# Kernel optimization log

Hardware: AMD Instinct MI355X
Metric: run time of the kernel (lower is better)

## Reference

```python
import jax, jax.numpy as jnp
import numpy as np

UNITS = 256
IN_DIM = 128
BATCH = 128
SEQ = 1024


def setup_inputs() -> dict:
    key = jax.random.key(0)
    k1, k2, k3 = jax.random.split(key, 3)
    x = jax.random.normal(k1, (BATCH, SEQ, IN_DIM), jnp.float32)
    # glorot-ish scale for stability
    input_weight = jax.random.normal(k2, (IN_DIM, 7 * UNITS), jnp.float32) * 0.05
    hidden_weight = jax.random.normal(k3, (UNITS, 3 * UNITS), jnp.float32) * 0.05
    bias = jnp.zeros((3 * UNITS,), jnp.float32)
    # constant = [eye(in_dim); zeros] of shape (units, in_dim), non-trainable
    constant = jnp.concatenate(
        [jnp.eye(IN_DIM, dtype=jnp.float32),
         jnp.zeros((UNITS - IN_DIM, IN_DIM), jnp.float32)], axis=0)
    return {"x": x, "input_weight": input_weight, "hidden_weight": hidden_weight,
            "bias": bias, "constant": constant}


def reference(x, input_weight, hidden_weight, bias, constant):
    u = hidden_weight.shape[0]
    Wxr, Wxu, Wxh, dWxr, dWxu, ddWxr, ddWxu = (
        [input_weight[:, i * u:(i + 1) * u] for i in range(7)])
    Whr, Whu, Whh = [hidden_weight[:, i * u:(i + 1) * u] for i in range(3)]
    br, bu, bh = bias[:u], bias[u:2 * u], bias[2 * u:]

    B = x.shape[0]
    h0 = jnp.zeros((B, u), x.dtype)
    s0 = jnp.zeros((B, u), x.dtype)

    def step(carry, x_t):
        h, s1, s2 = carry
        # recover padded previous inputs: (b,units) @ (units,in) -> (b,in)
        x_tm1 = s1 @ constant
        x_tm2 = s2 @ constant
        d_x = x_t - x_tm1                       # 1st-order finite diff
        dd_x = x_t - 2.0 * x_tm1 + x_tm2        # 2nd-order finite diff
        r = jax.nn.sigmoid(x_t @ Wxr + d_x @ dWxr + dd_x @ ddWxr + h @ Whr + br)
        ug = jax.nn.sigmoid(x_t @ Wxu + d_x @ dWxu + dd_x @ ddWxu + h @ Whu + bu)
        cand = jnp.tanh(x_t @ Wxh + (r * h) @ Whh + bh)
        h_new = ug * h + (1.0 - ug) * cand
        new_s1 = x_t @ constant.T               # pad x_t to units dims
        new_s2 = x_tm1 @ constant.T             # pad x_tm1 to units dims
        return (h_new, new_s1, new_s2), h_new

    xs = jnp.swapaxes(x, 0, 1)                  # (T, B, in_dim)
    _, hs = jax.lax.scan(step, (h0, s0, s0), xs)
    return jnp.swapaxes(hs, 0, 1)               # (B, T, units)
```

## Files before the change

### kernel.cpp

```cpp
#include <hip/hip_runtime.h>

#define SEQL 1024
#define BATCHN 128
#define UNITS 256
#define INDIM 128
#define G3 768

typedef __attribute__((ext_vector_type(8))) short short8;
typedef __attribute__((ext_vector_type(4))) short short4v;
typedef __attribute__((ext_vector_type(4))) float floatx4;

#define NL2E  -1.4426950408889634f
#define PL2E2  2.8853900817779268f

#define HSTRIDE 272

__device__ __forceinline__ short f2bf(float f) {
  unsigned u = __float_as_uint(f);
  u += 0x7fff + ((u >> 16) & 1);
  return (short)(u >> 16);
}
__device__ __forceinline__ float bf2f(unsigned short s) {
  return __uint_as_float(((unsigned)s) << 16);
}
__device__ __forceinline__ float fexp2(float x) {
#if __has_builtin(__builtin_amdgcn_exp2f)
  return __builtin_amdgcn_exp2f(x);
#else
  return __expf(0.6931471805599453f * x);
#endif
}
__device__ __forceinline__ float frcp(float x) {
#if __has_builtin(__builtin_amdgcn_rcpf)
  return __builtin_amdgcn_rcpf(x);
#else
  return 1.f / x;
#endif
}

#define LDS_BARRIER() do {                                   \
    asm volatile("s_waitcnt lgkmcnt(0)" ::: "memory");       \
    __builtin_amdgcn_s_barrier();                            \
    asm volatile("" ::: "memory");                           \
  } while (0)

__device__ __forceinline__ void acq_spin(const int* p) {
  while (__hip_atomic_load(p, __ATOMIC_ACQUIRE, __HIP_MEMORY_SCOPE_AGENT) == 0)
    __builtin_amdgcn_s_sleep(8);
}

__global__ void prep_kernel(const float* __restrict__ iw,
                            const float* __restrict__ hw,
                            short* __restrict__ WcB, short* __restrict__ WhB,
                            int* __restrict__ flags) {
  int idx = blockIdx.x * 256 + threadIdx.x;
  const int WCN = 384 * G3;
  if (idx < WCN) {
    int k = idx / G3, n = idx % G3;
    int i = k & 127, blkk = k >> 7;
    int gsel = n >> 8, c = n & 255;
    const float* row = iw + (size_t)i * 1792;
    float v;
    if (blkk == 0) {
      v = (gsel == 0) ? row[c] + row[768 + c] + row[1280 + c]
        : (gsel == 1) ? row[256 + c] + row[1024 + c] + row[1536 + c]
                      : row[512 + c];
    } else if (blkk == 1) {
      v = (gsel == 0) ? -(row[768 + c] + 2.f * row[1280 + c])
        : (gsel == 1) ? -(row[1024 + c] + 2.f * row[1536 + c])
                      : 0.f;
    } else {
      v = (gsel == 0) ? row[1280 + c]
        : (gsel == 1) ? row[1536 + c]
                      : 0.f;
    }
    v *= (gsel == 2) ? PL2E2 : NL2E;
    int kk = k >> 5, q = (k >> 3) & 3, j = k & 7;
    WcB[(((n * 12 + kk) * 4 + q) * 8) + j] = f2bf(v);
  } else {
    idx -= WCN;
    if (idx < 256 * G3) {
      int k = idx / G3, n = idx % G3;
      float v = hw[(size_t)k * G3 + n] * ((n >> 8) == 2 ? PL2E2 : NL2E);
      int kk = k >> 5, q = (k >> 3) & 3, j = k & 7;
      WhB[(((n * 8 + kk) * 4 + q) * 8) + j] = f2bf(v);
    } else {
      idx -= 256 * G3;
      if (idx < SEQL * 8) flags[idx] = 0;
    }
  }
}

__global__ __launch_bounds__(512, 2) void fused_kernel(
    const float* __restrict__ x, const short* __restrict__ WcB,
    const float* __restrict__ bias, unsigned* __restrict__ pre2,
    const short* __restrict__ WhB, float* __restrict__ out,
    int* __restrict__ flags) {
  __shared__ __align__(16) short smem[12288];

  if (blockIdx.x >= 32) {
    const int pidx = blockIdx.x - 32;
    const int tpair = pidx >> 3, mt = pidx & 7;
    const int tid = threadIdx.x;
    const int half = tid >> 8, htid = tid & 255;
    const int t = tpair * 2 + half;
    short* xF = smem + half * 6144;

#pragma unroll
    for (int it = 0; it < 6; ++it) {
      int rr = it * 8 + (htid >> 5);
      int dt = rr >> 4, bb = rr & 15;
      int lane32 = htid & 31, c = lane32 * 4;
      floatx4 v = {0.f, 0.f, 0.f, 0.f};
      if (t >= dt)
        v = *(const floatx4*)(x + ((size_t)(mt * 16 + bb) * SEQL + (t - dt)) * INDIM + c);
      int kk = dt * 4 + (c >> 5), qq = (c >> 3) & 3, j0 = c & 7;
      short4v pk;
#pragma unroll
      for (int j = 0; j < 4; ++j) pk[j] = f2bf(v[j]);
      *(short4v*)&xF[((kk * 64 + qq * 16 + bb) * 8) + j0] = pk;
    }
    __syncthreads();

    const int wvp = htid >> 6, lane = htid & 63, ln16 = lane & 15;
    const int qp = lane >> 4;

    short8 aF[12];
#pragma unroll
    for (int kk = 0; kk < 12; ++kk) aF[kk] = *(const short8*)&xF[(kk * 64 + lane) * 8];

    unsigned* slab = pre2 + (size_t)((mt * 4 + qp) * SEQL + t) * 1536;

#pragma unroll
    for (int ig = 0; ig < 3; ++ig) {
      const int ngrp = wvp * 3 + ig;
      const float sc = (ngrp >= 8) ? PL2E2 : NL2E;
      floatx4 acc[4];
#pragma unroll
      for (int nt = 0; nt < 4; ++nt) {
        float bv = bias[ngrp * 64 + nt * 16 + ln16] * sc;
#pragma unroll
        for (int r = 0; r < 4; ++r) acc[nt][r] = bv;
      }
#pragma unroll
      for (int kk = 0; kk < 12; ++kk) {
#pragma unroll
        for (int nt = 0; nt < 4; ++nt) {
          int n = ngrp * 64 + nt * 16 + ln16;
          short8 w = *(const short8*)(WcB + (((size_t)(n * 12 + kk) * 4 + qp) * 8));
          acc[nt] = __builtin_amdgcn_mfma_f32_16x16x32_bf16(aF[kk], w, acc[nt], 0, 0, 0);
        }
      }
      const int g = ngrp >> 2;
#pragma unroll
      for (int p = 0; p < 2; ++p) {
        int wvc = (ngrp & 3) * 2 + p;
#pragma unroll
        for (int r = 0; r < 4; ++r) {
          unsigned lo = (unsigned)(unsigned short)f2bf(acc[2 * p][r]);
          unsigned hi = (unsigned)(unsigned short)f2bf(acc[2 * p + 1][r]);
          slab[g * 512 + wvc * 64 + r * 16 + ln16] = lo | (hi << 16);
        }
      }
    }

    __syncthreads();
    if (tid == 0) {
      __threadfence();
      __hip_atomic_store(&flags[(2 * tpair) * 8 + mt], 1,
                         __ATOMIC_RELEASE, __HIP_MEMORY_SCOPE_AGENT);
      __hip_atomic_store(&flags[(2 * tpair + 1) * 8 + mt], 1,
                         __ATOMIC_RELEASE, __HIP_MEMORY_SCOPE_AGENT);
    }
    return;
  }

  short* hFc = smem;
  short* rFc = smem + 4 * HSTRIDE;

  const int tid = threadIdx.x;
  const int wv = tid >> 6, lane = tid & 63, ln16 = lane & 15, q = lane >> 4;
  const int row4 = lane & 3;
  const int wg = blockIdx.x;
  const int mtg = wg >> 2;

  short8 wR[2][8], wU[2][8], wH[2][8];
#pragma unroll
  for (int nt = 0; nt < 2; ++nt) {
    int nr = wv * 32 + nt * 16 + ln16;
#pragma unroll
    for (int kk = 0; kk < 8; ++kk) {
      wR[nt][kk] = *(const short8*)(WhB + (((size_t)(nr * 8 + kk) * 4 + q) * 8));
      wU[nt][kk] = *(const short8*)(WhB + (((size_t)((256 + nr) * 8 + kk) * 4 + q) * 8));
      wH[nt][kk] = *(const short8*)(WhB + (((size_t)((512 + nr) * 8 + kk) * 4 + q) * 8));
    }
  }
  for (int i = tid; i < 4 * HSTRIDE; i += 512) { hFc[i] = 0; rFc[i] = 0; }

  const floatx4 z4 = {0.f, 0.f, 0.f, 0.f};
  float hq[2] = {0.f, 0.f};

  const unsigned* slab0 = pre2 + (size_t)wg * SEQL * 1536;

  acq_spin(&flags[0 * 8 + mtg]);
  unsigned cur0 = slab0[0 * 512 + tid];
  unsigned cur1 = slab0[1 * 512 + tid];
  unsigned cur2 = slab0[2 * 512 + tid];
  int fcur = __hip_atomic_load(&flags[1 * 8 + mtg],
                               __ATOMIC_RELAXED, __HIP_MEMORY_SCOPE_AGENT);

  float* outBase = out + ((size_t)(wg * 4 + q) * SEQL) * UNITS + wv * 32 + ln16;
  const int aoff = row4 * HSTRIDE + q * 8;
  const int woff = q * HSTRIDE + wv * 32 + ln16;

  __syncthreads();

  for (int t = 0; t < SEQL; ++t) {
    int fnxt = 1;
    if (t + 2 < SEQL)
      fnxt = __hip_atomic_load(&flags[(t + 2) * 8 + mtg],
                               __ATOMIC_RELAXED, __HIP_MEMORY_SCOPE_AGENT);
    if (t + 1 < SEQL && fcur == 0) acq_spin(&flags[(t + 1) * 8 + mtg]);
    asm volatile("" ::: "memory");

    const unsigned* nslab = slab0 + (size_t)(t < SEQL - 1 ? t + 1 : t) * 1536;
    unsigned nxt0 = nslab[0 * 512 + tid];
    unsigned nxt1 = nslab[1 * 512 + tid];
    unsigned nxt2 = nslab[2 * 512 + tid];

    floatx4 accR[2], accU[2];
    {
      const short8 a0 = *(const short8*)&hFc[aoff];
      accR[0] = __builtin_amdgcn_mfma_f32_16x16x32_bf16(a0, wR[0][0], z4, 0, 0, 0);
      accR[1] = __builtin_amdgcn_mfma_f32_16x16x32_bf16(a0, wR[1][0], z4, 0, 0, 0);
      accU[0] = __builtin_amdgcn_mfma_f32_16x16x32_bf16(a0, wU[0][0], z4, 0, 0, 0);
      accU[1] = __builtin_amdgcn_mfma_f32_16x16x32_bf16(a0, wU[1][0], z4, 0, 0, 0);
    }
#pragma unroll
    for (int kk = 1; kk < 8; ++kk) {
      const short8 a = *(const short8*)&hFc[aoff + kk * 32];
      accR[0] = __builtin_amdgcn_mfma_f32_16x16x32_bf16(a, wR[0][kk], accR[0], 0, 0, 0);
      accR[1] = __builtin_amdgcn_mfma_f32_16x16x32_bf16(a, wR[1][kk], accR[1], 0, 0, 0);
      accU[0] = __builtin_amdgcn_mfma_f32_16x16x32_bf16(a, wU[0][kk], accU[0], 0, 0, 0);
      accU[1] = __builtin_amdgcn_mfma_f32_16x16x32_bf16(a, wU[1][kk], accU[1], 0, 0, 0);
    }
    float uq[2];
#pragma unroll
    for (int nt = 0; nt < 2; ++nt) {
      float vR = (q == 0) ? accR[nt][0] : (q == 1) ? accR[nt][1]
               : (q == 2) ? accR[nt][2] : accR[nt][3];
      float vU = (q == 0) ? accU[nt][0] : (q == 1) ? accU[nt][1]
               : (q == 2) ? accU[nt][2] : accU[nt][3];
      float pR = bf2f((unsigned short)(nt ? (cur0 >> 16) : (cur0 & 0xffff)));
      float pU = bf2f((unsigned short)(nt ? (cur1 >> 16) : (cur1 & 0xffff)));
      float rg = frcp(1.f + fexp2(vR + pR));
      uq[nt]   = frcp(1.f + fexp2(vU + pU));
      rFc[woff + nt * 16] = f2bf(rg * hq[nt]);
    }
    LDS_BARRIER();

    floatx4 accH[2];
    {
      const short8 a0 = *(const short8*)&rFc[aoff];
      accH[0] = __builtin_amdgcn_mfma_f32_16x16x32_bf16(a0, wH[0][0], z4, 0, 0, 0);
      accH[1] = __builtin_amdgcn_mfma_f32_16x16x32_bf16(a0, wH[1][0], z4, 0, 0, 0);
    }
#pragma unroll
    for (int kk = 1; kk < 8; ++kk) {
      const short8 a = *(const short8*)&rFc[aoff + kk * 32];
      accH[0] = __builtin_amdgcn_mfma_f32_16x16x32_bf16(a, wH[0][kk], accH[0], 0, 0, 0);
      accH[1] = __builtin_amdgcn_mfma_f32_16x16x32_bf16(a, wH[1][kk], accH[1], 0, 0, 0);
    }
#pragma unroll
    for (int nt = 0; nt < 2; ++nt) {
      float vH = (q == 0) ? accH[nt][0] : (q == 1) ? accH[nt][1]
               : (q == 2) ? accH[nt][2] : accH[nt][3];
      float pH = bf2f((unsigned short)(nt ? (cur2 >> 16) : (cur2 & 0xffff)));
      float cand = 1.f - 2.f * frcp(1.f + fexp2(vH + pH));
      float hnew = uq[nt] * (hq[nt] - cand) + cand;
      hq[nt] = hnew;
      hFc[woff + nt * 16] = f2bf(hnew);
      outBase[(size_t)t * UNITS + nt * 16] = hnew;
    }
    cur0 = nxt0; cur1 = nxt1; cur2 = nxt2; fcur = fnxt;
    LDS_BARRIER();
  }
}

extern "C" void kernel_launch(void* const* d_in, const int* in_sizes, int n_in,
                              void* d_out, int out_size, void* d_ws, size_t ws_size,
                              hipStream_t stream) {
  const float* x    = (const float*)d_in[0];
  const float* iw   = (const float*)d_in[1];
  const float* hw   = (const float*)d_in[2];
  const float* bias = (const float*)d_in[3];
  float* out = (float*)d_out;

  unsigned* pre2 = (unsigned*)d_ws;
  const size_t preDwords = (size_t)32 * SEQL * 1536;
  short* WcB = (short*)(pre2 + preDwords);
  short* WhB = WcB + (size_t)384 * G3;
  int* flags = (int*)(WhB + (size_t)256 * G3);

  prep_kernel<<<1952, 256, 0, stream>>>(iw, hw, WcB, WhB, flags);
  fused_kernel<<<32 + 4096, 512, 0, stream>>>(x, WcB, bias, pre2, WhB, out, flags);
}
```

Before: 1.574 ms.

## Restructure input projection blocks to one timestep across all batch tiles

```diff
diff --git a/kernel.cpp b/kernel.cpp
--- a/kernel.cpp
+++ b/kernel.cpp
@@ -86,80 +86,82 @@
       WhB[(((n * 8 + kk) * 4 + q) * 8) + j] = f2bf(v);
     } else {
       idx -= 256 * G3;
-      if (idx < SEQL * 8) flags[idx] = 0;
-    }
-  }
-}
-
-__global__ __launch_bounds__(512, 2) void fused_kernel(
+      if (idx < SEQL) flags[idx] = 0;
+    }
+  }
+}
+
+__global__ __launch_bounds__(512, 1) void fused_kernel(
     const float* __restrict__ x, const short* __restrict__ WcB,
     const float* __restrict__ bias, unsigned* __restrict__ pre2,
     const short* __restrict__ WhB, float* __restrict__ out,
     int* __restrict__ flags) {
-  __shared__ __align__(16) short smem[12288];
+  __shared__ __align__(16) short xA[6144 * 8];
+  __shared__ __align__(16) short hFc[4 * HSTRIDE];
+  __shared__ __align__(16) short rFc[4 * HSTRIDE];
+
+  const int tid = threadIdx.x;
 
   if (blockIdx.x >= 32) {
-    const int pidx = blockIdx.x - 32;
-    const int tpair = pidx >> 3, mt = pidx & 7;
-    const int tid = threadIdx.x;
-    const int half = tid >> 8, htid = tid & 255;
-    const int t = tpair * 2 + half;
-    short* xF = smem + half * 6144;
-
-#pragma unroll
-    for (int it = 0; it < 6; ++it) {
-      int rr = it * 8 + (htid >> 5);
-      int dt = rr >> 4, bb = rr & 15;
-      int lane32 = htid & 31, c = lane32 * 4;
-      floatx4 v = {0.f, 0.f, 0.f, 0.f};
-      if (t >= dt)
-        v = *(const floatx4*)(x + ((size_t)(mt * 16 + bb) * SEQL + (t - dt)) * INDIM + c);
-      int kk = dt * 4 + (c >> 5), qq = (c >> 3) & 3, j0 = c & 7;
-      short4v pk;
-#pragma unroll
-      for (int j = 0; j < 4; ++j) pk[j] = f2bf(v[j]);
-      *(short4v*)&xF[((kk * 64 + qq * 16 + bb) * 8) + j0] = pk;
+    const int t = blockIdx.x - 32;
+
+#pragma unroll
+    for (int it = 0; it < 12; ++it) {
+      int u = it * 512 + tid;
+      int kk8mi = u >> 6, l6 = u & 63;
+      int kk = kk8mi >> 3, mi = kk8mi & 7;
+      int qq = l6 >> 4, bb = l6 & 15;
+      int row = mi * 16 + bb;
+      int k = kk * 32 + qq * 8;
+      int dt = k >> 7, kin = k & 127;
+      floatx4 v0 = {0.f, 0.f, 0.f, 0.f}, v1 = {0.f, 0.f, 0.f, 0.f};
+      if (t >= dt) {
+        const float* src = x + ((size_t)row * SEQL + (t - dt)) * INDIM + kin;
+        v0 = *(const floatx4*)src;
+        v1 = *(const floatx4*)(src + 4);
+      }
+      short8 pk;
+#pragma unroll
+      for (int j = 0; j < 4; ++j) { pk[j] = f2bf(v0[j]); pk[4 + j] = f2bf(v1[j]); }
+      *(short8*)&xA[u * 8] = pk;
     }
     __syncthreads();
 
-    const int wvp = htid >> 6, lane = htid & 63, ln16 = lane & 15;
-    const int qp = lane >> 4;
-
-    short8 aF[12];
-#pragma unroll
-    for (int kk = 0; kk < 12; ++kk) aF[kk] = *(const short8*)&xF[(kk * 64 + lane) * 8];
-
-    unsigned* slab = pre2 + (size_t)((mt * 4 + qp) * SEQL + t) * 1536;
-
-#pragma unroll
-    for (int ig = 0; ig < 3; ++ig) {
-      const int ngrp = wvp * 3 + ig;
-      const float sc = (ngrp >= 8) ? PL2E2 : NL2E;
-      floatx4 acc[4];
-#pragma unroll
-      for (int nt = 0; nt < 4; ++nt) {
-        float bv = bias[ngrp * 64 + nt * 16 + ln16] * sc;
-#pragma unroll
-        for (int r = 0; r < 4; ++r) acc[nt][r] = bv;
+    const int w = tid >> 6, lane = tid & 63, ln16 = lane & 15, qp = lane >> 4;
+
+#pragma unroll
+    for (int j = 0; j < 3; ++j) {
+      const int n0 = w * 96 + 32 * j;
+      const int nA = n0 + ln16, nB = n0 + 16 + ln16;
+      const int g = n0 >> 8;
+      const float sc = (g == 2) ? PL2E2 : NL2E;
+      const int wvc = (n0 & 255) >> 5;
+
+      short8 wA[12], wB[12];
+#pragma unroll
+      for (int kk = 0; kk < 12; ++kk) {
+        wA[kk] = *(const short8*)(WcB + (((size_t)(nA * 12 + kk) * 4 + qp) * 8));
+        wB[kk] = *(const short8*)(WcB + (((size_t)(nB * 12 + kk) * 4 + qp) * 8));
       }
-#pragma unroll
-      for (int kk = 0; kk < 12; ++kk) {
-#pragma unroll
-        for (int nt = 0; nt < 4; ++nt) {
-          int n = ngrp * 64 + nt * 16 + ln16;
-          short8 w = *(const short8*)(WcB + (((size_t)(n * 12 + kk) * 4 + qp) * 8));
-          acc[nt] = __builtin_amdgcn_mfma_f32_16x16x32_bf16(aF[kk], w, acc[nt], 0, 0, 0);
+      const float bvA = bias[nA] * sc, bvB = bias[nB] * sc;
+
+#pragma unroll
+      for (int mi = 0; mi < 8; ++mi) {
+        floatx4 aA = {bvA, bvA, bvA, bvA};
+        floatx4 aB = {bvB, bvB, bvB, bvB};
+#pragma unroll
+        for (int kk = 0; kk < 12; ++kk) {
+          const short8 a = *(const short8*)&xA[(((kk * 8 + mi) * 64) + lane) * 8];
+          aA = __builtin_amdgcn_mfma_f32_16x16x32_bf16(a, wA[kk], aA, 0, 0, 0);
+          aB = __builtin_amdgcn_mfma_f32_16x16x32_bf16(a, wB[kk], aB, 0, 0, 0);
         }
-      }
-      const int g = ngrp >> 2;
-#pragma unroll
-      for (int p = 0; p < 2; ++p) {
-        int wvc = (ngrp & 3) * 2 + p;
+        unsigned* slab = pre2 + (size_t)((mi * 4 + qp) * SEQL + t) * 1536
+                       + g * 512 + wvc * 64 + ln16;
 #pragma unroll
         for (int r = 0; r < 4; ++r) {
-          unsigned lo = (unsigned)(unsigned short)f2bf(acc[2 * p][r]);
-          unsigned hi = (unsigned)(unsigned short)f2bf(acc[2 * p + 1][r]);
-          slab[g * 512 + wvc * 64 + r * 16 + ln16] = lo | (hi << 16);
+          unsigned lo = (unsigned)(unsigned short)f2bf(aA[r]);
+          unsigned hi = (unsigned)(unsigned short)f2bf(aB[r]);
+          slab[r * 16] = lo | (hi << 16);
         }
       }
     }
@@ -167,22 +169,14 @@
     __syncthreads();
     if (tid == 0) {
       __threadfence();
-      __hip_atomic_store(&flags[(2 * tpair) * 8 + mt], 1,
-                         __ATOMIC_RELEASE, __HIP_MEMORY_SCOPE_AGENT);
-      __hip_atomic_store(&flags[(2 * tpair + 1) * 8 + mt], 1,
-                         __ATOMIC_RELEASE, __HIP_MEMORY_SCOPE_AGENT);
+      __hip_atomic_store(&flags[t], 1, __ATOMIC_RELEASE, __HIP_MEMORY_SCOPE_AGENT);
     }
     return;
   }
 
-  short* hFc = smem;
-  short* rFc = smem + 4 * HSTRIDE;
-
-  const int tid = threadIdx.x;
   const int wv = tid >> 6, lane = tid & 63, ln16 = lane & 15, q = lane >> 4;
   const int row4 = lane & 3;
   const int wg = blockIdx.x;
-  const int mtg = wg >> 2;
 
   short8 wR[2][8], wU[2][8], wH[2][8];
 #pragma unroll
@@ -202,12 +196,11 @@
 
   const unsigned* slab0 = pre2 + (size_t)wg * SEQL * 1536;
 
-  acq_spin(&flags[0 * 8 + mtg]);
+  acq_spin(&flags[0]);
   unsigned cur0 = slab0[0 * 512 + tid];
   unsigned cur1 = slab0[1 * 512 + tid];
   unsigned cur2 = slab0[2 * 512 + tid];
-  int fcur = __hip_atomic_load(&flags[1 * 8 + mtg],
-                               __ATOMIC_RELAXED, __HIP_MEMORY_SCOPE_AGENT);
+  int fcur = __hip_atomic_load(&flags[1], __ATOMIC_RELAXED, __HIP_MEMORY_SCOPE_AGENT);
 
   float* outBase = out + ((size_t)(wg * 4 + q) * SEQL) * UNITS + wv * 32 + ln16;
   const int aoff = row4 * HSTRIDE + q * 8;
@@ -218,9 +211,8 @@
   for (int t = 0; t < SEQL; ++t) {
     int fnxt = 1;
     if (t + 2 < SEQL)
-      fnxt = __hip_atomic_load(&flags[(t + 2) * 8 + mtg],
-                               __ATOMIC_RELAXED, __HIP_MEMORY_SCOPE_AGENT);
-    if (t + 1 < SEQL && fcur == 0) acq_spin(&flags[(t + 1) * 8 + mtg]);
+      fnxt = __hip_atomic_load(&flags[t + 2], __ATOMIC_RELAXED, __HIP_MEMORY_SCOPE_AGENT);
+    if (t + 1 < SEQL && fcur == 0) acq_spin(&flags[t + 1]);
     asm volatile("" ::: "memory");
 
     const unsigned* nslab = slab0 + (size_t)(t < SEQL - 1 ? t + 1 : t) * 1536;
@@ -303,5 +295,5 @@
   int* flags = (int*)(WhB + (size_t)256 * G3);
 
   prep_kernel<<<1952, 256, 0, stream>>>(iw, hw, WcB, WhB, flags);
-  fused_kernel<<<32 + 4096, 512, 0, stream>>>(x, WcB, bias, pre2, WhB, out, flags);
-}
+  fused_kernel<<<32 + 1024, 512, 0, stream>>>(x, WcB, bias, pre2, WhB, out, flags);
+}
```

Result: faster. 1.407 ms (-10.6%).
